# Kernel optimization log

Hardware: AMD Instinct MI355X
Metric: run time of the kernel (lower is better)

## Reference

```python
import jax, jax.numpy as jnp
import numpy as np

# irrep multiplicities: 32x0e + 16x1o + 16x1e + 8x0o  -> feature size 32+48+48+8 = 136
M0E, M1O, M1E, M0O = 32, 16, 16, 8
FEAT = M0E + 3 * M1O + 3 * M1E + M0O  # 136
WS = {'0e': (M0E + M1O, M0E), '1o': (M0E + M1O + M1E, M1O), '1e': (M1O + M1E + M0O, M1E), '0o': (M1E + M0O, M0O)}
WNUM = sum(a * b for a, b in WS.values())  # 3392
N_NODES, N_EDGES, EDGE_FEAT, HIDDEN = 8192, 65536, 64, 64


def setup_inputs() -> dict:
    key = jax.random.key(0)
    ks = jax.random.split(key, 8)
    return {
        'node_attr': jax.random.normal(ks[0], (N_NODES, FEAT), jnp.float32),
        'edge_index': jax.random.randint(ks[1], (2, N_EDGES), 0, N_NODES),
        'edge_attr': jax.random.normal(ks[2], (N_EDGES, EDGE_FEAT), jnp.float32),
        'edge_sh': jax.random.normal(ks[3], (N_EDGES, 4), jnp.float32),
        'fc_w1': jax.random.normal(ks[4], (EDGE_FEAT, HIDDEN), jnp.float32) / np.sqrt(EDGE_FEAT),
        'fc_b1': jnp.zeros((HIDDEN,), jnp.float32),
        'fc_w2': jax.random.normal(ks[5], (HIDDEN, WNUM), jnp.float32) / np.sqrt(HIDDEN),
        'fc_b2': jnp.zeros((WNUM,), jnp.float32),
    }


def reference(node_attr, edge_index, edge_attr, edge_sh, fc_w1, fc_b1, fc_w2, fc_b2):
    N = node_attr.shape[0]
    src, dst = edge_index[0], edge_index[1]
    # per-edge tensor-product weights via 2-layer MLP (FCBlock, relu)
    w = jax.nn.relu(edge_attr @ fc_w1 + fc_b1) @ fc_w2 + fc_b2  # [E, WNUM]
    x = node_attr[dst]                                          # gather [E, 136]
    x0e = x[:, :M0E]
    x1o = x[:, M0E:M0E + 3 * M1O].reshape(-1, M1O, 3)
    x1e = x[:, M0E + 3 * M1O:M0E + 3 * M1O + 3 * M1E].reshape(-1, M1E, 3)
    x0o = x[:, -M0O:]
    sh0, sh1 = edge_sh[:, 0], edge_sh[:, 1:4]
    inv_s3, inv_s2 = 1.0 / np.sqrt(3.0), 1.0 / np.sqrt(2.0)
    # uncoupled tensor-product outputs per output irrep
    o0e = jnp.concatenate([x0e * sh0[:, None],
                           (x1o * sh1[:, None, :]).sum(-1) * inv_s3], axis=-1)           # [E,48]
    o1o = jnp.concatenate([x0e[:, :, None] * sh1[:, None, :],
                           x1o * sh0[:, None, None],
                           jnp.cross(x1e, sh1[:, None, :]) * inv_s2], axis=1)            # [E,64,3]
    o1e = jnp.concatenate([jnp.cross(x1o, sh1[:, None, :]) * inv_s2,
                           x1e * sh0[:, None, None],
                           x0o[:, :, None] * sh1[:, None, :]], axis=1)                   # [E,40,3]
    o0o = jnp.concatenate([(x1e * sh1[:, None, :]).sum(-1) * inv_s3,
                           x0o * sh0[:, None]], axis=-1)                                 # [E,24]
    # per-edge weight slices, normalized by sqrt(fan_in)
    off = 0
    wd = {}
    for k in ('0e', '1o', '1e', '0o'):
        i, o = WS[k]
        wd[k] = w[:, off:off + i * o].reshape(-1, i, o) / np.sqrt(i)
        off += i * o
    y0e = jnp.einsum('ei,eio->eo', o0e, wd['0e'])
    y1o = jnp.einsum('eic,eio->eoc', o1o, wd['1o']).reshape(-1, 3 * M1O)
    y1e = jnp.einsum('eic,eio->eoc', o1e, wd['1e']).reshape(-1, 3 * M1E)
    y0o = jnp.einsum('ei,eio->eo', o0o, wd['0o'])
    tp = jnp.concatenate([y0e, y1o, y1e, y0o], axis=-1)  # [E,136]
    # scatter-mean to source nodes
    summed = jax.ops.segment_sum(tp, src, num_segments=N)
    cnt = jax.ops.segment_sum(jnp.ones((tp.shape[0],), tp.dtype), src, num_segments=N)
    out = summed / jnp.maximum(cnt, 1.0)[:, None]
    # residual (out_irreps == in_irreps, so no padding needed)
    return out + node_attr
```

## Files before the change

kernel.cpp:

```cpp
#include <hip/hip_runtime.h>

#define N_NODES 8192
#define N_EDGES 65536
#define FEAT    136
#define WNUM    3392

typedef __attribute__((ext_vector_type(4))) short s16x4;
typedef __attribute__((ext_vector_type(8))) short s16x8;
typedef __attribute__((ext_vector_type(4))) float f32x4;
typedef __attribute__((ext_vector_type(2))) float f32x2;

__device__ __forceinline__ float b2f(unsigned short h) {
    union { unsigned int u; float f; } v; v.u = ((unsigned int)h) << 16; return v.f;
}
__device__ __forceinline__ unsigned short f2b(float f) {
    union { float f; unsigned int u; } v; v.f = f;
    unsigned int u = v.u;
    unsigned int r = (u + 0x7FFFu + ((u >> 16) & 1u)) >> 16;
    return (unsigned short)r;
}

__device__ __forceinline__ float wscale(int col) {
    const float inv_s3 = 0.57735026918962576f;
    const float inv_s2 = 0.70710678118654752f;
    if (col < 1536) { int i = col >> 5;          return 0.14433756729740643f * (i < 32 ? 1.f : inv_s3); }
    if (col < 2560) { int i = (col - 1536) >> 4; return 0.125f               * (i >= 48 ? inv_s2 : 1.f); }
    if (col < 3200) { int i = (col - 2560) >> 4; return 0.15811388300841897f * (i < 16 ? inv_s2 : 1.f); }
    {               int i = (col - 3200) >> 3;   return 0.20412414523193150f * (i < 16 ? inv_s3 : 1.f); }
}

__global__ void transpose_kernel(const float* __restrict__ w2,
                                 const float* __restrict__ w1,
                                 const float* __restrict__ bias2,
                                 unsigned short* __restrict__ w2t,
                                 unsigned short* __restrict__ w1t,
                                 float* __restrict__ b2s,
                                 float* __restrict__ zero_base) {
    __shared__ float tl[64 * 65];
    const int b = blockIdx.x, tid = threadIdx.x;
    if (b >= 54) {
        int idx = (b - 54) * 256 + tid;
        float4 z = {0.f, 0.f, 0.f, 0.f};
        if (idx < 280576) ((float4*)zero_base)[idx] = z;
        return;
    }
    if (b < 53) {
        const int c0 = b * 64;
        for (int idx = tid; idx < 4096; idx += 256) {
            int k = idx >> 6, c = idx & 63;
            tl[c * 65 + k] = w2[k * WNUM + c0 + c];
        }
        __syncthreads();
        for (int idx = tid; idx < 4096; idx += 256) {
            int fl   = idx >> 10;
            int rem  = idx & 1023;
            int half = rem >> 9;
            int ln   = (rem >> 3) & 63;
            int j    = idx & 7;
            int q = ln >> 4, nn = ln & 15;
            int cl  = fl * 16 + nn;
            int k   = half * 32 + q * 8 + j;
            int col = c0 + cl;
            w2t[(size_t)b * 4096 + idx] = f2b(tl[cl * 65 + k] * wscale(col));
        }
        if (tid < 64) {
            int col = c0 + tid;
            b2s[col] = bias2[col] * wscale(col);
        }
    } else {
        for (int idx = tid; idx < 4096; idx += 256) {
            int k = idx >> 6, j = idx & 63;
            tl[j * 65 + k] = w1[k * 64 + j];
        }
        __syncthreads();
        for (int idx = tid; idx < 4096; idx += 256) {
            int j = idx >> 6, k = idx & 63;
            w1t[j * 64 + k] = f2b(tl[j * 65 + k]);
        }
    }
}

__device__ __forceinline__ void gload_lds16(const unsigned short* g, unsigned short* l) {
    __builtin_amdgcn_global_load_lds(
        (const __attribute__((address_space(1))) unsigned int*)g,
        (__attribute__((address_space(3))) unsigned int*)l, 16, 0, 0);
}

__global__ __launch_bounds__(256, 4)
void tpconv_main(const float* __restrict__ node_attr,
                 const int* __restrict__ edge_index,
                 const float* __restrict__ edge_attr,
                 const float* __restrict__ edge_sh,
                 const unsigned short* __restrict__ w1t,
                 const float* __restrict__ b1,
                 const unsigned short* __restrict__ w2t,
                 const float* __restrict__ b2s,
                 float* __restrict__ acc_g,
                 float* __restrict__ cnt_g) {
    __shared__ __align__(16) char smem[37632];
    unsigned short* x_lds = (unsigned short*)smem;
    unsigned short* wbuf  = (unsigned short*)(smem + 18944);
    unsigned short* h_lds = (unsigned short*)(smem + 18944);
    float* sh_lds = (float*)(smem + 28160);
    int* dst_lds  = (int*)(smem + 29184);
    int* src_lds  = (int*)(smem + 37120);

    const int tid  = threadIdx.x;
    const int lane = tid & 63;
    const int wv   = tid >> 6;
    const int n    = lane & 15;
    const int quad = lane >> 4;
    const int eb   = blockIdx.x * 64;

    if (tid < 64) {
        int s = edge_index[eb + tid];
        int d = edge_index[N_EDGES + eb + tid];
        src_lds[tid] = s;
        dst_lds[tid] = d;
        atomicAdd(&cnt_g[s], 1.0f);
        const float4 shv = *(const float4*)&edge_sh[(size_t)(eb + tid) * 4];
        sh_lds[tid * 4 + 0] = shv.x;
        sh_lds[tid * 4 + 1] = shv.y;
        sh_lds[tid * 4 + 2] = shv.z;
        sh_lds[tid * 4 + 3] = shv.w;
    }
    {
        const float* ea = edge_attr + (size_t)(eb + wv * 16 + n) * 64 + quad * 8;
        s16x8 a0, a1;
#pragma unroll
        for (int j = 0; j < 8; ++j) {
            a0[j] = (short)f2b(ea[j]);
            a1[j] = (short)f2b(ea[32 + j]);
        }
        for (int ct = 0; ct < 4; ++ct) {
            int col = ct * 16 + n;
            const unsigned short* wp = w1t + col * 64;
            s16x8 bu0 = *(const s16x8*)&wp[quad * 8];
            s16x8 bu1 = *(const s16x8*)&wp[32 + quad * 8];
            f32x4 acc = {0.f, 0.f, 0.f, 0.f};
            acc = __builtin_amdgcn_mfma_f32_16x16x32_bf16(a0, bu0, acc, 0, 0, 0);
            acc = __builtin_amdgcn_mfma_f32_16x16x32_bf16(a1, bu1, acc, 0, 0, 0);
            float bias = b1[col];
            for (int r = 0; r < 4; ++r) {
                float hv = acc[r] + bias;
                hv = hv > 0.f ? hv : 0.f;
                h_lds[(wv * 16 + quad * 4 + r) * 72 + col] = f2b(hv);
            }
        }
    }
    __syncthreads();

    for (int idx = tid; idx < 64 * 34; idx += 256) {
        int e = idx / 34, seg = idx - e * 34;
        const float4 v = *(const float4*)(node_attr + (size_t)dst_lds[e] * FEAT + seg * 4);
        s16x4 pk;
        pk[0] = (short)f2b(v.x); pk[1] = (short)f2b(v.y);
        pk[2] = (short)f2b(v.z); pk[3] = (short)f2b(v.w);
        *(s16x4*)&x_lds[e * 148 + seg * 4] = pk;
    }
    const int eLoc = wv * 16 + n;
    const float sh0 = sh_lds[eLoc * 4 + 0];
    const float s1x = sh_lds[eLoc * 4 + 1];
    const float s1y = sh_lds[eLoc * 4 + 2];
    const float s1z = sh_lds[eLoc * 4 + 3];
    const unsigned short* hp = &h_lds[eLoc * 72];
    s16x8 h0 = *(const s16x8*)&hp[quad * 8];
    s16x8 h1 = *(const s16x8*)&hp[32 + quad * 8];
    const unsigned short* xr = &x_lds[eLoc * 148];

    __syncthreads();

    {
        const unsigned short* g = w2t + (wv << 10) + (lane << 3);
        unsigned short* l = wbuf + (wv << 10);
        gload_lds16(g, l);
        gload_lds16(g + 512, l + 512);
    }
    f32x4 bvv[4];
#pragma unroll
    for (int t = 0; t < 4; ++t)
        bvv[t] = *(const f32x4*)(b2s + 16 * t + quad * 4);

    f32x2 Y0e2[2][2] = {};
    f32x2 Y1o2[2][3] = {};
    f32x2 Y1e2[2][3] = {};
    f32x2 Y0o2[2]    = {};

#define CHUNK_TOP(c)                                                          \
    __syncthreads();                                                          \
    if ((c) < 52) {                                                           \
        const unsigned short* g = w2t + (((size_t)(c) + 1) << 12) + (wv << 10) + (lane << 3); \
        unsigned short* l = wbuf + ((((c) + 1) & 1) << 12) + (wv << 10);      \
        gload_lds16(g, l);                                                    \
        gload_lds16(g + 512, l + 512);                                        \
    }                                                                         \
    const unsigned short* cb = wbuf + (((c) & 1) << 12);

#define CHUNK_REFILL(c)                                                       \
    if ((c) < 52) {                                                           \
        _Pragma("unroll")                                                     \
        for (int t = 0; t < 4; ++t)                                           \
            bvv[t] = *(const f32x4*)(b2s + ((c) + 1) * 64 + 16 * t + quad * 4); \
    }

#define MFMA_T(t)                                                             \
    const unsigned short* bp = cb + (t) * 1024 + (lane << 3);                 \
    s16x8 aT0 = *(const s16x8*)bp;                                            \
    s16x8 aT1 = *(const s16x8*)(bp + 512);                                    \
    f32x4 acc = bvv[t];                                                       \
    acc = __builtin_amdgcn_mfma_f32_16x16x32_bf16(aT0, h0, acc, 0, 0, 0);     \
    acc = __builtin_amdgcn_mfma_f32_16x16x32_bf16(aT1, h1, acc, 0, 0, 0);     \
    f32x2 a01 = {acc[0], acc[1]}; f32x2 a23 = {acc[2], acc[3]};

#define ACC3(Y)                                                               \
    Y[0][0] += a01 * o0; Y[1][0] += a23 * o0;                                 \
    Y[0][1] += a01 * o1; Y[1][1] += a23 * o1;                                 \
    Y[0][2] += a01 * o2; Y[1][2] += a23 * o2;

    for (int c = 0; c < 16; ++c) {
        CHUNK_TOP(c)
        float ov = 0.f;
#pragma unroll
        for (int t = 0; t < 4; ++t) {
            MFMA_T(t)
            if ((t & 1) == 0) ov = b2f(xr[2 * c + (t >> 1)]) * sh0;
            const int kk = t & 1;
            Y0e2[0][kk] += a01 * ov;
            Y0e2[1][kk] += a23 * ov;
        }
        CHUNK_REFILL(c)
    }
    for (int c = 16; c < 24; ++c) {
        CHUNK_TOP(c)
        float ov = 0.f;
#pragma unroll
        for (int t = 0; t < 4; ++t) {
            MFMA_T(t)
            if ((t & 1) == 0) {
                int ib = 32 + 3 * (2 * c + (t >> 1) - 32);
                ov = b2f(xr[ib]) * s1x + b2f(xr[ib + 1]) * s1y + b2f(xr[ib + 2]) * s1z;
            }
            const int kk = t & 1;
            Y0e2[0][kk] += a01 * ov;
            Y0e2[1][kk] += a23 * ov;
        }
        CHUNK_REFILL(c)
    }
    for (int c = 24; c < 32; ++c) {
        CHUNK_TOP(c)
#pragma unroll
        for (int t = 0; t < 4; ++t) {
            MFMA_T(t)
            float xv = b2f(xr[4 * (c - 24) + t]);
            float o0 = xv * s1x, o1 = xv * s1y, o2 = xv * s1z;
            ACC3(Y1o2)
        }
        CHUNK_REFILL(c)
    }
    for (int c = 32; c < 36; ++c) {
        CHUNK_TOP(c)
#pragma unroll
        for (int t = 0; t < 4; ++t) {
            MFMA_T(t)
            int ib = 32 + 3 * (4 * (c - 24) + t - 32);
            float o0 = b2f(xr[ib]) * sh0, o1 = b2f(xr[ib + 1]) * sh0, o2 = b2f(xr[ib + 2]) * sh0;
            ACC3(Y1o2)
        }
        CHUNK_REFILL(c)
    }
    for (int c = 36; c < 40; ++c) {
        CHUNK_TOP(c)
#pragma unroll
        for (int t = 0; t < 4; ++t) {
            MFMA_T(t)
            int ib = 80 + 3 * (4 * (c - 24) + t - 48);
            float a0v = b2f(xr[ib]), a1v = b2f(xr[ib + 1]), a2v = b2f(xr[ib + 2]);
            float o0 = a1v * s1z - a2v * s1y;
            float o1 = a2v * s1x - a0v * s1z;
            float o2 = a0v * s1y - a1v * s1x;
            ACC3(Y1o2)
        }
        CHUNK_REFILL(c)
    }
    for (int c = 40; c < 44; ++c) {
        CHUNK_TOP(c)
#pragma unroll
        for (int t = 0; t < 4; ++t) {
            MFMA_T(t)
            int ib = 32 + 3 * (4 * (c - 40) + t);
            float a0v = b2f(xr[ib]), a1v = b2f(xr[ib + 1]), a2v = b2f(xr[ib + 2]);
            float o0 = a1v * s1z - a2v * s1y;
            float o1 = a2v * s1x - a0v * s1z;
            float o2 = a0v * s1y - a1v * s1x;
            ACC3(Y1e2)
        }
        CHUNK_REFILL(c)
    }
    for (int c = 44; c < 48; ++c) {
        CHUNK_TOP(c)
#pragma unroll
        for (int t = 0; t < 4; ++t) {
            MFMA_T(t)
            int ib = 80 + 3 * (4 * (c - 40) + t - 16);
            float o0 = b2f(xr[ib]) * sh0, o1 = b2f(xr[ib + 1]) * sh0, o2 = b2f(xr[ib + 2]) * sh0;
            ACC3(Y1e2)
        }
        CHUNK_REFILL(c)
    }
    for (int c = 48; c < 50; ++c) {
        CHUNK_TOP(c)
#pragma unroll
        for (int t = 0; t < 4; ++t) {
            MFMA_T(t)
            float xv = b2f(xr[128 + (4 * (c - 40) + t - 32)]);
            float o0 = xv * s1x, o1 = xv * s1y, o2 = xv * s1z;
            ACC3(Y1e2)
        }
        CHUNK_REFILL(c)
    }
    for (int c = 50; c < 52; ++c) {
        CHUNK_TOP(c)
#pragma unroll
        for (int t = 0; t < 4; ++t) {
            MFMA_T(t)
            int ib = 80 + 3 * (8 * (c - 50) + 2 * t + (quad >> 1));
            float ov = b2f(xr[ib]) * s1x + b2f(xr[ib + 1]) * s1y + b2f(xr[ib + 2]) * s1z;
            Y0o2[0] += a01 * ov;
            Y0o2[1] += a23 * ov;
        }
        CHUNK_REFILL(c)
    }
    {
        CHUNK_TOP(52)
#pragma unroll
        for (int t = 0; t < 4; ++t) {
            MFMA_T(t)
            float ov = b2f(xr[128 + 2 * t + (quad >> 1)]) * sh0;
            Y0o2[0] += a01 * ov;
            Y0o2[1] += a23 * ov;
        }
    }
#undef ACC3
#undef MFMA_T
#undef CHUNK_TOP
#undef CHUNK_REFILL

    __syncthreads();
    float* stage = (float*)smem;
    {
        float* srow = stage + eLoc * 145;
#pragma unroll
        for (int r = 0; r < 4; ++r) {
            const int p = r >> 1, s = r & 1;
            int qr = quad * 4 + r;
            srow[qr]              = Y0e2[p][0][s];
            srow[16 + qr]         = Y0e2[p][1][s];
            srow[32 + qr * 3 + 0] = Y1o2[p][0][s];
            srow[32 + qr * 3 + 1] = Y1o2[p][1][s];
            srow[32 + qr * 3 + 2] = Y1o2[p][2][s];
            srow[80 + qr * 3 + 0] = Y1e2[p][0][s];
            srow[80 + qr * 3 + 1] = Y1e2[p][1][s];
            srow[80 + qr * 3 + 2] = Y1e2[p][2][s];
            srow[128 + (quad & 1) * 4 + r + (quad >> 1) * 8] = Y0o2[p][s];
        }
    }
    __syncthreads();
    for (int j = 0; j < 16; ++j) {
        int e = wv * 16 + j;
        float* dp = acc_g + (size_t)src_lds[e] * FEAT;
        const float* sr = stage + e * 145;
        atomicAdd(dp + lane,      sr[lane]);
        atomicAdd(dp + 64 + lane, sr[64 + lane]);
        if (lane < 8)
            atomicAdd(dp + 128 + lane, sr[128 + lane] + sr[136 + lane]);
    }
}

__global__ void finalize_kernel(const float* __restrict__ acc_g,
                                const float* __restrict__ cnt_g,
                                const float* __restrict__ node_attr,
                                float* __restrict__ out) {
    int idx = blockIdx.x * 256 + threadIdx.x;
    if (idx >= N_NODES * FEAT) return;
    int nn = idx / FEAT;
    float c = cnt_g[nn];
    out[idx] = acc_g[idx] / fmaxf(c, 1.0f) + node_attr[idx];
}

extern "C" void kernel_launch(void* const* d_in, const int* in_sizes, int n_in,
                              void* d_out, int out_size, void* d_ws, size_t ws_size,
                              hipStream_t stream) {
    const float* node_attr  = (const float*)d_in[0];
    const int*   edge_index = (const int*)d_in[1];
    const float* edge_attr  = (const float*)d_in[2];
    const float* edge_sh    = (const float*)d_in[3];
    const float* fc_w1      = (const float*)d_in[4];
    const float* fc_b1      = (const float*)d_in[5];
    const float* fc_w2      = (const float*)d_in[6];
    const float* fc_b2      = (const float*)d_in[7];
    float* out = (float*)d_out;

    char* ws = (char*)d_ws;
    float* acc_g = (float*)ws;
    float* cnt_g = (float*)(ws + 4456448);
    unsigned short* w2t = (unsigned short*)(ws + 4489216);
    unsigned short* w1t = (unsigned short*)(ws + 4489216 + 434176);
    float* b2s = (float*)(ws + 4489216 + 434176 + 8192);

    transpose_kernel<<<1150, 256, 0, stream>>>(fc_w2, fc_w1, fc_b2, w2t, w1t, b2s, acc_g);
    tpconv_main<<<1024, 256, 0, stream>>>(node_attr, edge_index, edge_attr, edge_sh,
                                          w1t, fc_b1, w2t, b2s, acc_g, cnt_g);
    finalize_kernel<<<(N_NODES * FEAT + 255) / 256, 256, 0, stream>>>(acc_g, cnt_g, node_attr, out);
}
```

Baseline: 167.1 us.

## Split W2 column tiles across two wave groups with 512-thread blocks

After: 174.5 us. 4.4% more time.

```diff
diff --git a/kernel.cpp b/kernel.cpp
--- a/kernel.cpp
+++ b/kernel.cpp
@@ -86,7 +86,7 @@
         (__attribute__((address_space(3))) unsigned int*)l, 16, 0, 0);
 }
 
-__global__ __launch_bounds__(256, 4)
+__global__ __launch_bounds__(512, 4)
 void tpconv_main(const float* __restrict__ node_attr,
                  const int* __restrict__ edge_index,
                  const float* __restrict__ edge_attr,
@@ -110,6 +110,8 @@
     const int wv   = tid >> 6;
     const int n    = lane & 15;
     const int quad = lane >> 4;
+    const int et   = wv & 3;
+    const int ch   = wv >> 2;
     const int eb   = blockIdx.x * 64;
 
     if (tid < 64) {
@@ -125,15 +127,16 @@
         sh_lds[tid * 4 + 3] = shv.w;
     }
     {
-        const float* ea = edge_attr + (size_t)(eb + wv * 16 + n) * 64 + quad * 8;
+        const float* ea = edge_attr + (size_t)(eb + et * 16 + n) * 64 + quad * 8;
         s16x8 a0, a1;
 #pragma unroll
         for (int j = 0; j < 8; ++j) {
             a0[j] = (short)f2b(ea[j]);
             a1[j] = (short)f2b(ea[32 + j]);
         }
-        for (int ct = 0; ct < 4; ++ct) {
-            int col = ct * 16 + n;
+#pragma unroll
+        for (int c2 = 0; c2 < 2; ++c2) {
+            int col = (2 * ch + c2) * 16 + n;
             const unsigned short* wp = w1t + col * 64;
             s16x8 bu0 = *(const s16x8*)&wp[quad * 8];
             s16x8 bu1 = *(const s16x8*)&wp[32 + quad * 8];
@@ -144,13 +147,13 @@
             for (int r = 0; r < 4; ++r) {
                 float hv = acc[r] + bias;
                 hv = hv > 0.f ? hv : 0.f;
-                h_lds[(wv * 16 + quad * 4 + r) * 72 + col] = f2b(hv);
+                h_lds[(et * 16 + quad * 4 + r) * 72 + col] = f2b(hv);
             }
         }
     }
     __syncthreads();
 
-    for (int idx = tid; idx < 64 * 34; idx += 256) {
+    for (int idx = tid; idx < 64 * 34; idx += 512) {
         int e = idx / 34, seg = idx - e * 34;
         const float4 v = *(const float4*)(node_attr + (size_t)dst_lds[e] * FEAT + seg * 4);
         s16x4 pk;
@@ -158,7 +161,7 @@
         pk[2] = (short)f2b(v.z); pk[3] = (short)f2b(v.w);
         *(s16x4*)&x_lds[e * 148 + seg * 4] = pk;
     }
-    const int eLoc = wv * 16 + n;
+    const int eLoc = et * 16 + n;
     const float sh0 = sh_lds[eLoc * 4 + 0];
     const float s1x = sh_lds[eLoc * 4 + 1];
     const float s1y = sh_lds[eLoc * 4 + 2];
@@ -171,15 +174,13 @@
     __syncthreads();
 
     {
-        const unsigned short* g = w2t + (wv << 10) + (lane << 3);
-        unsigned short* l = wbuf + (wv << 10);
-        gload_lds16(g, l);
-        gload_lds16(g + 512, l + 512);
-    }
-    f32x4 bvv[4];
-#pragma unroll
-    for (int t = 0; t < 4; ++t)
-        bvv[t] = *(const f32x4*)(b2s + 16 * t + quad * 4);
+        const unsigned short* g = w2t + (wv << 9) + (lane << 3);
+        gload_lds16(g, wbuf + (wv << 9));
+    }
+    f32x4 bvv[2];
+#pragma unroll
+    for (int b = 0; b < 2; ++b)
+        bvv[b] = *(const f32x4*)(b2s + (2 * ch + b) * 16 + quad * 4);
 
     f32x2 Y0e2[2][2] = {};
     f32x2 Y1o2[2][3] = {};
@@ -189,27 +190,27 @@
 #define CHUNK_TOP(c)                                                          \
     __syncthreads();                                                          \
     if ((c) < 52) {                                                           \
-        const unsigned short* g = w2t + (((size_t)(c) + 1) << 12) + (wv << 10) + (lane << 3); \
-        unsigned short* l = wbuf + ((((c) + 1) & 1) << 12) + (wv << 10);      \
-        gload_lds16(g, l);                                                    \
-        gload_lds16(g + 512, l + 512);                                        \
+        const unsigned short* g = w2t + (((size_t)(c) + 1) << 12) + (wv << 9) + (lane << 3); \
+        gload_lds16(g, wbuf + ((((c) + 1) & 1) << 12) + (wv << 9));           \
     }                                                                         \
-    const unsigned short* cb = wbuf + (((c) & 1) << 12);
+    const unsigned short* cb = wbuf + (((c) & 1) << 12) + (ch << 11) + (lane << 3); \
+    s16x8 Afr[4];                                                             \
+    Afr[0] = *(const s16x8*)(cb);                                             \
+    Afr[1] = *(const s16x8*)(cb + 512);                                       \
+    Afr[2] = *(const s16x8*)(cb + 1024);                                      \
+    Afr[3] = *(const s16x8*)(cb + 1536);
 
 #define CHUNK_REFILL(c)                                                       \
     if ((c) < 52) {                                                           \
         _Pragma("unroll")                                                     \
-        for (int t = 0; t < 4; ++t)                                           \
-            bvv[t] = *(const f32x4*)(b2s + ((c) + 1) * 64 + 16 * t + quad * 4); \
-    }
-
-#define MFMA_T(t)                                                             \
-    const unsigned short* bp = cb + (t) * 1024 + (lane << 3);                 \
-    s16x8 aT0 = *(const s16x8*)bp;                                            \
-    s16x8 aT1 = *(const s16x8*)(bp + 512);                                    \
-    f32x4 acc = bvv[t];                                                       \
-    acc = __builtin_amdgcn_mfma_f32_16x16x32_bf16(aT0, h0, acc, 0, 0, 0);     \
-    acc = __builtin_amdgcn_mfma_f32_16x16x32_bf16(aT1, h1, acc, 0, 0, 0);     \
+        for (int b = 0; b < 2; ++b)                                           \
+            bvv[b] = *(const f32x4*)(b2s + ((c) + 1) * 64 + (2 * ch + b) * 16 + quad * 4); \
+    }
+
+#define MFMA_T(b)                                                             \
+    f32x4 acc = bvv[b];                                                       \
+    acc = __builtin_amdgcn_mfma_f32_16x16x32_bf16(Afr[2 * (b)], h0, acc, 0, 0, 0);     \
+    acc = __builtin_amdgcn_mfma_f32_16x16x32_bf16(Afr[2 * (b) + 1], h1, acc, 0, 0, 0); \
     f32x2 a01 = {acc[0], acc[1]}; f32x2 a23 = {acc[2], acc[3]};
 
 #define ACC3(Y)                                                               \
@@ -219,39 +220,33 @@
 
     for (int c = 0; c < 16; ++c) {
         CHUNK_TOP(c)
-        float ov = 0.f;
-#pragma unroll
-        for (int t = 0; t < 4; ++t) {
-            MFMA_T(t)
-            if ((t & 1) == 0) ov = b2f(xr[2 * c + (t >> 1)]) * sh0;
-            const int kk = t & 1;
-            Y0e2[0][kk] += a01 * ov;
-            Y0e2[1][kk] += a23 * ov;
+        const float ov = b2f(xr[2 * c + ch]) * sh0;
+#pragma unroll
+        for (int b = 0; b < 2; ++b) {
+            MFMA_T(b)
+            Y0e2[0][b] += a01 * ov;
+            Y0e2[1][b] += a23 * ov;
         }
         CHUNK_REFILL(c)
     }
     for (int c = 16; c < 24; ++c) {
         CHUNK_TOP(c)
-        float ov = 0.f;
-#pragma unroll
-        for (int t = 0; t < 4; ++t) {
-            MFMA_T(t)
-            if ((t & 1) == 0) {
-                int ib = 32 + 3 * (2 * c + (t >> 1) - 32);
-                ov = b2f(xr[ib]) * s1x + b2f(xr[ib + 1]) * s1y + b2f(xr[ib + 2]) * s1z;
-            }
-            const int kk = t & 1;
-            Y0e2[0][kk] += a01 * ov;
-            Y0e2[1][kk] += a23 * ov;
+        int ib = 32 + 3 * (2 * c + ch - 32);
+        const float ov = b2f(xr[ib]) * s1x + b2f(xr[ib + 1]) * s1y + b2f(xr[ib + 2]) * s1z;
+#pragma unroll
+        for (int b = 0; b < 2; ++b) {
+            MFMA_T(b)
+            Y0e2[0][b] += a01 * ov;
+            Y0e2[1][b] += a23 * ov;
         }
         CHUNK_REFILL(c)
     }
     for (int c = 24; c < 32; ++c) {
         CHUNK_TOP(c)
 #pragma unroll
-        for (int t = 0; t < 4; ++t) {
-            MFMA_T(t)
-            float xv = b2f(xr[4 * (c - 24) + t]);
+        for (int b = 0; b < 2; ++b) {
+            MFMA_T(b)
+            float xv = b2f(xr[4 * (c - 24) + 2 * ch + b]);
             float o0 = xv * s1x, o1 = xv * s1y, o2 = xv * s1z;
             ACC3(Y1o2)
         }
@@ -260,9 +255,9 @@
     for (int c = 32; c < 36; ++c) {
         CHUNK_TOP(c)
 #pragma unroll
-        for (int t = 0; t < 4; ++t) {
-            MFMA_T(t)
-            int ib = 32 + 3 * (4 * (c - 24) + t - 32);
+        for (int b = 0; b < 2; ++b) {
+            MFMA_T(b)
+            int ib = 32 + 3 * (4 * (c - 24) + 2 * ch + b - 32);
             float o0 = b2f(xr[ib]) * sh0, o1 = b2f(xr[ib + 1]) * sh0, o2 = b2f(xr[ib + 2]) * sh0;
             ACC3(Y1o2)
         }
@@ -271,9 +266,9 @@
     for (int c = 36; c < 40; ++c) {
         CHUNK_TOP(c)
 #pragma unroll
-        for (int t = 0; t < 4; ++t) {
-            MFMA_T(t)
-            int ib = 80 + 3 * (4 * (c - 24) + t - 48);
+        for (int b = 0; b < 2; ++b) {
+            MFMA_T(b)
+            int ib = 80 + 3 * (4 * (c - 24) + 2 * ch + b - 48);
             float a0v = b2f(xr[ib]), a1v = b2f(xr[ib + 1]), a2v = b2f(xr[ib + 2]);
             float o0 = a1v * s1z - a2v * s1y;
             float o1 = a2v * s1x - a0v * s1z;
@@ -285,9 +280,9 @@
     for (int c = 40; c < 44; ++c) {
         CHUNK_TOP(c)
 #pragma unroll
-        for (int t = 0; t < 4; ++t) {
-            MFMA_T(t)
-            int ib = 32 + 3 * (4 * (c - 40) + t);
+        for (int b = 0; b < 2; ++b) {
+            MFMA_T(b)
+            int ib = 32 + 3 * (4 * (c - 40) + 2 * ch + b);
             float a0v = b2f(xr[ib]), a1v = b2f(xr[ib + 1]), a2v = b2f(xr[ib + 2]);
             float o0 = a1v * s1z - a2v * s1y;
             float o1 = a2v * s1x - a0v * s1z;
@@ -299,9 +294,9 @@
     for (int c = 44; c < 48; ++c) {
         CHUNK_TOP(c)
 #pragma unroll
-        for (int t = 0; t < 4; ++t) {
-            MFMA_T(t)
-            int ib = 80 + 3 * (4 * (c - 40) + t - 16);
+        for (int b = 0; b < 2; ++b) {
+            MFMA_T(b)
+            int ib = 80 + 3 * (4 * (c - 40) + 2 * ch + b - 16);
             float o0 = b2f(xr[ib]) * sh0, o1 = b2f(xr[ib + 1]) * sh0, o2 = b2f(xr[ib + 2]) * sh0;
             ACC3(Y1e2)
         }
@@ -310,9 +305,9 @@
     for (int c = 48; c < 50; ++c) {
         CHUNK_TOP(c)
 #pragma unroll
-        for (int t = 0; t < 4; ++t) {
-            MFMA_T(t)
-            float xv = b2f(xr[128 + (4 * (c - 40) + t - 32)]);
+        for (int b = 0; b < 2; ++b) {
+            MFMA_T(b)
+            float xv = b2f(xr[128 + (4 * (c - 40) + 2 * ch + b - 32)]);
             float o0 = xv * s1x, o1 = xv * s1y, o2 = xv * s1z;
             ACC3(Y1e2)
         }
@@ -321,9 +316,9 @@
     for (int c = 50; c < 52; ++c) {
         CHUNK_TOP(c)
 #pragma unroll
-        for (int t = 0; t < 4; ++t) {
-            MFMA_T(t)
-            int ib = 80 + 3 * (8 * (c - 50) + 2 * t + (quad >> 1));
+        for (int b = 0; b < 2; ++b) {
+            MFMA_T(b)
+            int ib = 80 + 3 * (8 * (c - 50) + 4 * ch + 2 * b + (quad >> 1));
             float ov = b2f(xr[ib]) * s1x + b2f(xr[ib + 1]) * s1y + b2f(xr[ib + 2]) * s1z;
             Y0o2[0] += a01 * ov;
             Y0o2[1] += a23 * ov;
@@ -333,9 +328,9 @@
     {
         CHUNK_TOP(52)
 #pragma unroll
-        for (int t = 0; t < 4; ++t) {
-            MFMA_T(t)
-            float ov = b2f(xr[128 + 2 * t + (quad >> 1)]) * sh0;
+        for (int b = 0; b < 2; ++b) {
+            MFMA_T(b)
+            float ov = b2f(xr[128 + 4 * ch + 2 * b + (quad >> 1)]) * sh0;
             Y0o2[0] += a01 * ov;
             Y0o2[1] += a23 * ov;
         }
@@ -347,26 +342,32 @@
 
     __syncthreads();
     float* stage = (float*)smem;
-    {
-        float* srow = stage + eLoc * 145;
-#pragma unroll
-        for (int r = 0; r < 4; ++r) {
-            const int p = r >> 1, s = r & 1;
-            int qr = quad * 4 + r;
-            srow[qr]              = Y0e2[p][0][s];
-            srow[16 + qr]         = Y0e2[p][1][s];
-            srow[32 + qr * 3 + 0] = Y1o2[p][0][s];
-            srow[32 + qr * 3 + 1] = Y1o2[p][1][s];
-            srow[32 + qr * 3 + 2] = Y1o2[p][2][s];
-            srow[80 + qr * 3 + 0] = Y1e2[p][0][s];
-            srow[80 + qr * 3 + 1] = Y1e2[p][1][s];
-            srow[80 + qr * 3 + 2] = Y1e2[p][2][s];
-            srow[128 + (quad & 1) * 4 + r + (quad >> 1) * 8] = Y0o2[p][s];
-        }
-    }
+    float* srow = stage + eLoc * 145;
+
+#define EMIT(OPEQ)                                                            \
+    _Pragma("unroll")                                                         \
+    for (int r = 0; r < 4; ++r) {                                             \
+        const int p = r >> 1, s = r & 1;                                      \
+        int qr = quad * 4 + r;                                                \
+        srow[qr]              OPEQ Y0e2[p][0][s];                             \
+        srow[16 + qr]         OPEQ Y0e2[p][1][s];                             \
+        srow[32 + qr * 3 + 0] OPEQ Y1o2[p][0][s];                             \
+        srow[32 + qr * 3 + 1] OPEQ Y1o2[p][1][s];                             \
+        srow[32 + qr * 3 + 2] OPEQ Y1o2[p][2][s];                             \
+        srow[80 + qr * 3 + 0] OPEQ Y1e2[p][0][s];                             \
+        srow[80 + qr * 3 + 1] OPEQ Y1e2[p][1][s];                             \
+        srow[80 + qr * 3 + 2] OPEQ Y1e2[p][2][s];                             \
+        srow[128 + (quad & 1) * 4 + r + (quad >> 1) * 8] OPEQ Y0o2[p][s];     \
+    }
+
+    if (ch == 0) { EMIT(=) }
     __syncthreads();
-    for (int j = 0; j < 16; ++j) {
-        int e = wv * 16 + j;
+    if (ch == 1) { EMIT(+=) }
+#undef EMIT
+    __syncthreads();
+
+    for (int j = 0; j < 8; ++j) {
+        int e = wv * 8 + j;
         float* dp = acc_g + (size_t)src_lds[e] * FEAT;
         const float* sr = stage + e * 145;
         atomicAdd(dp + lane,      sr[lane]);
@@ -408,7 +409,7 @@
     float* b2s = (float*)(ws + 4489216 + 434176 + 8192);
 
     transpose_kernel<<<1150, 256, 0, stream>>>(fc_w2, fc_w1, fc_b2, w2t, w1t, b2s, acc_g);
-    tpconv_main<<<1024, 256, 0, stream>>>(node_attr, edge_index, edge_attr, edge_sh,
+    tpconv_main<<<1024, 512, 0, stream>>>(node_attr, edge_index, edge_attr, edge_sh,
                                           w1t, fc_b1, w2t, b2s, acc_g, cnt_g);
     finalize_kernel<<<(N_NODES * FEAT + 255) / 256, 256, 0, stream>>>(acc_g, cnt_g, node_attr, out);
 }
```
